# Kernel optimization log

Hardware: AMD Instinct MI355X
Metric: run time of the kernel (lower is better)

The kernel has to match this reference:

```python
import jax, jax.numpy as jnp
import numpy as np

DIM = 2048
H = 16        # num query heads
KVH = 4       # num kv heads
HD = DIM // H # head_dim = 128
RD = 64       # rope_dims (< head_dim -> partial rope)
BASE = 10000.0
SCALE = HD ** -0.5
EPS_RMS = 1e-6
EPS_NORM = 1e-12


def _rms_norm(x):
    return x * jax.lax.rsqrt(jnp.mean(x * x, axis=-1, keepdims=True) + EPS_RMS)


def _rope_cache(T):
    inv_freq = 1.0 / (BASE ** (jnp.arange(0, RD, 2, dtype=jnp.float32) / RD))  # [RD/2]
    t = jnp.arange(T, dtype=jnp.float32)
    freqs = t[:, None] * inv_freq[None, :]  # [T, RD/2]
    return jnp.cos(freqs)[None, None], jnp.sin(freqs)[None, None]  # [1,1,T,RD/2]


def _apply_rope(x, cos, sin):
    # x: [B, H, T, HD]; rotate first RD dims, pass through the rest
    x_rope, x_pass = x[..., :RD], x[..., RD:]
    half = RD // 2
    x1, x2 = x_rope[..., :half], x_rope[..., half:]
    x_rot = jnp.concatenate([x1 * cos - x2 * sin, x2 * cos + x1 * sin], axis=-1)
    return jnp.concatenate([x_rot, x_pass], axis=-1)


def setup_inputs() -> dict:
    key = jax.random.key(0)
    ks = jax.random.split(key, 6)
    x = jax.random.normal(ks[0], (4, 2048, DIM), dtype=jnp.float32)
    Wq = jax.random.normal(ks[1], (DIM, DIM), dtype=jnp.float32) * 0.02
    Wk = jax.random.normal(ks[2], (KVH * HD, DIM), dtype=jnp.float32) * 0.02
    Wv = jax.random.normal(ks[3], (KVH * HD, DIM), dtype=jnp.float32) * 0.02
    Wproj = jax.random.normal(ks[4], (DIM, DIM), dtype=jnp.float32) * 0.02
    q_gain = jnp.ones((H,), dtype=jnp.float32)
    return {"x": x, "Wq": Wq, "Wk": Wk, "Wv": Wv, "Wproj": Wproj, "q_gain": q_gain}


def reference(x, Wq, Wk, Wv, Wproj, q_gain):
    B, T, _ = x.shape
    # projections (nn.Linear: x @ W.T)  ->  [B, heads, T, HD]
    q = (x @ Wq.T).reshape(B, T, H, HD).transpose(0, 2, 1, 3)
    k = (x @ Wk.T).reshape(B, T, KVH, HD).transpose(0, 2, 1, 3)
    v = (x @ Wv.T).reshape(B, T, KVH, HD).transpose(0, 2, 1, 3)

    cos, sin = _rope_cache(T)
    q = _apply_rope(_rms_norm(q), cos, sin) * q_gain[None, :, None, None]
    k = _apply_rope(_rms_norm(k), cos, sin)

    # GQA: expand kv heads (kv head i serves query heads i*rep .. i*rep+rep-1)
    rep = H // KVH
    k = jnp.repeat(k, rep, axis=1)      # [B, H, T, HD]
    v_attn = jnp.repeat(v, rep, axis=1)  # [B, H, T, HD]

    # causal SDPA
    scores = jnp.einsum("bhqd,bhkd->bhqk", q, k) * SCALE
    causal = jnp.tril(jnp.ones((T, T), dtype=bool))
    scores = jnp.where(causal[None, None], scores, jnp.finfo(scores.dtype).min)
    attn = jax.nn.softmax(scores, axis=-1)
    y = jnp.einsum("bhqk,bhkd->bhqd", attn, v_attn)

    # xsa postproc: remove component of y along unit value direction
    vn = v_attn / jnp.maximum(
        jnp.linalg.norm(v_attn, axis=-1, keepdims=True), EPS_NORM)
    y = y - jnp.sum(y * vn, axis=-1, keepdims=True) * vn

    y = y.transpose(0, 2, 1, 3).reshape(B, T, DIM)
    return y @ Wproj.T
```

## Files before the change

kernel.cpp:

```cpp
#include <hip/hip_runtime.h>
#include <cstdint>
#include <cstddef>

typedef __bf16 bf16_t;
typedef __bf16 bf16x4 __attribute__((ext_vector_type(4)));
typedef __bf16 bf16x8 __attribute__((ext_vector_type(8)));
typedef float f32x4 __attribute__((ext_vector_type(4)));

#define B_ 4
#define T_ 2048
#define DIM_ 2048
#define H_ 16
#define KVH_ 4
#define HD_ 128
#define QKV_ 3072
#define QSCALE (0.08838834764831845f * 1.4426950408889634f)

__device__ __forceinline__ void gload16(const bf16_t* g, bf16_t* l) {
  __builtin_amdgcn_global_load_lds(
      (const __attribute__((address_space(1))) unsigned int*)g,
      (__attribute__((address_space(3))) unsigned int*)l, 16, 0, 0);
}

__global__ __launch_bounds__(256) void cvt_all(const float4* __restrict__ x,
                                               const float4* __restrict__ wq,
                                               const float4* __restrict__ wk,
                                               const float4* __restrict__ wv,
                                               const float4* __restrict__ wp,
                                               bf16x4* __restrict__ xb,
                                               bf16x4* __restrict__ wqkvb,
                                               bf16x4* __restrict__ wpb) {
  int i = blockIdx.x * 256 + threadIdx.x;
  const float4* s;
  bf16x4* dst;
  int off;
  if (i < 4194304) { s = x; dst = xb; off = i; }
  else if (i < 5242880) { s = wq; dst = wqkvb; off = i - 4194304; }
  else if (i < 5505024) { s = wk; dst = wqkvb + 1048576; off = i - 5242880; }
  else if (i < 5767168) { s = wv; dst = wqkvb + 1310720; off = i - 5505024; }
  else { s = wp; dst = wpb; off = i - 5767168; }
  float4 v = s[off];
  bf16x4 o = {(__bf16)v.x, (__bf16)v.y, (__bf16)v.z, (__bf16)v.w};
  dst[off] = o;
}

#define STAGE2(gsrc, ldst)                                   \
  do {                                                       \
    gload16((gsrc), (ldst) + tid * 8);                       \
    gload16((gsrc) + (size_t)128 * K, (ldst) + 4096 + tid * 8); \
  } while (0)

__global__ __launch_bounds__(512, 2) void gemm_bt(const bf16_t* __restrict__ A,
                                                  const bf16_t* __restrict__ B,
                                                  void* __restrict__ Cp,
                                                  int M, int N, int K, int out_bf16) {
  __shared__ __align__(16) bf16_t Ab[2 * 16384];
  __shared__ __align__(16) bf16_t Bb[2 * 16384];
  const int tid = threadIdx.x;
  const int w = tid >> 6, lane = tid & 63;
  const int m16 = lane & 15, q4 = lane >> 4;
  const int wr = w >> 2, wc = w & 3;
  const int rowBase = blockIdx.y * 256, colBase = blockIdx.x * 256;

  const int srow = tid >> 2, skc = tid & 3;
  const bf16_t* srcA = A + (size_t)(rowBase + srow) * K + (skc ^ (srow & 3)) * 8;
  const bf16_t* srcB = B + (size_t)(colBase + srow) * K + (skc ^ (srow & 3)) * 8;

  const int cs = (q4 ^ m16) & 3;
  const int aoff = wr * 4096 + m16 * 32 + cs * 8;
  const int boff = wc * 2048 + m16 * 32 + cs * 8;

  f32x4 acc[8][4];
#pragma unroll
  for (int i = 0; i < 8; ++i)
#pragma unroll
    for (int j = 0; j < 4; ++j) acc[i][j] = (f32x4){0.f, 0.f, 0.f, 0.f};

  const int nt = K >> 6;
  STAGE2(srcA, Ab);
  STAGE2(srcB, Bb);
  STAGE2(srcA + 32, Ab + 8192);
  STAGE2(srcB + 32, Bb + 8192);
  asm volatile("s_waitcnt vmcnt(4)" ::: "memory");
  __builtin_amdgcn_s_barrier();

#pragma unroll 1
  for (int t = 0; t < nt; ++t) {
    const int cb = (t & 1) << 14, nb = cb ^ 16384;
    const int pk = ((t + 1 < nt) ? t + 1 : t) << 6;
    const bf16_t* Ac = Ab + cb + aoff;
    const bf16_t* Bc = Bb + cb + boff;
    bf16x8 a[4], b[4];

    STAGE2(srcA + pk, Ab + nb);
#pragma unroll
    for (int i = 0; i < 4; ++i) a[i] = *(const bf16x8*)(Ac + i * 512);
#pragma unroll
    for (int j = 0; j < 4; ++j) b[j] = *(const bf16x8*)(Bc + j * 512);
    __builtin_amdgcn_s_barrier();
    asm volatile("s_waitcnt lgkmcnt(0)" ::: "memory");
    __builtin_amdgcn_sched_barrier(0);
    __builtin_amdgcn_s_setprio(1);
#pragma unroll
    for (int i = 0; i < 4; ++i)
#pragma unroll
      for (int j = 0; j < 4; ++j)
        acc[i][j] = __builtin_amdgcn_mfma_f32_16x16x32_bf16(a[i], b[j], acc[i][j], 0, 0, 0);
    __builtin_amdgcn_s_setprio(0);
    __builtin_amdgcn_s_barrier();

    STAGE2(srcB + pk, Bb + nb);
#pragma unroll
    for (int i = 0; i < 4; ++i) a[i] = *(const bf16x8*)(Ac + (4 + i) * 512);
    __builtin_amdgcn_s_barrier();
    asm volatile("s_waitcnt lgkmcnt(0)" ::: "memory");
    __builtin_amdgcn_sched_barrier(0);
    __builtin_amdgcn_s_setprio(1);
#pragma unroll
    for (int i = 0; i < 4; ++i)
#pragma unroll
      for (int j = 0; j < 4; ++j)
        acc[4 + i][j] = __builtin_amdgcn_mfma_f32_16x16x32_bf16(a[i], b[j], acc[4 + i][j], 0, 0, 0);
    __builtin_amdgcn_s_setprio(0);
    asm volatile("s_waitcnt vmcnt(4)" ::: "memory");
    __builtin_amdgcn_s_barrier();

    STAGE2(srcA + pk + 32, Ab + nb + 8192);
#pragma unroll
    for (int i = 0; i < 4; ++i) a[i] = *(const bf16x8*)(Ac + 8192 + i * 512);
#pragma unroll
    for (int j = 0; j < 4; ++j) b[j] = *(const bf16x8*)(Bc + 8192 + j * 512);
    __builtin_amdgcn_s_barrier();
    asm volatile("s_waitcnt lgkmcnt(0)" ::: "memory");
    __builtin_amdgcn_sched_barrier(0);
    __builtin_amdgcn_s_setprio(1);
#pragma unroll
    for (int i = 0; i < 4; ++i)
#pragma unroll
      for (int j = 0; j < 4; ++j)
        acc[i][j] = __builtin_amdgcn_mfma_f32_16x16x32_bf16(a[i], b[j], acc[i][j], 0, 0, 0);
    __builtin_amdgcn_s_setprio(0);
    __builtin_amdgcn_s_barrier();

    STAGE2(srcB + pk + 32, Bb + nb + 8192);
#pragma unroll
    for (int i = 0; i < 4; ++i) a[i] = *(const bf16x8*)(Ac + 8192 + (4 + i) * 512);
    __builtin_amdgcn_s_barrier();
    asm volatile("s_waitcnt lgkmcnt(0)" ::: "memory");
    __builtin_amdgcn_sched_barrier(0);
    __builtin_amdgcn_s_setprio(1);
#pragma unroll
    for (int i = 0; i < 4; ++i)
#pragma unroll
      for (int j = 0; j < 4; ++j)
        acc[4 + i][j] = __builtin_amdgcn_mfma_f32_16x16x32_bf16(a[i], b[j], acc[4 + i][j], 0, 0, 0);
    __builtin_amdgcn_s_setprio(0);
    asm volatile("s_waitcnt vmcnt(4)" ::: "memory");
    __builtin_amdgcn_s_barrier();
  }

  if (out_bf16) {
    bf16_t* C = (bf16_t*)Cp;
#pragma unroll
    for (int i = 0; i < 8; ++i)
#pragma unroll
      for (int j = 0; j < 4; ++j)
#pragma unroll
        for (int r = 0; r < 4; ++r) {
          int row = rowBase + wr * 128 + i * 16 + q4 * 4 + r;
          int col = colBase + wc * 64 + j * 16 + m16;
          C[(size_t)row * N + col] = (bf16_t)acc[i][j][r];
        }
  } else {
    float* C = (float*)Cp;
#pragma unroll
    for (int i = 0; i < 8; ++i)
#pragma unroll
      for (int j = 0; j < 4; ++j)
#pragma unroll
        for (int r = 0; r < 4; ++r) {
          int row = rowBase + wr * 128 + i * 16 + q4 * 4 + r;
          int col = colBase + wc * 64 + j * 16 + m16;
          C[(size_t)row * N + col] = acc[i][j][r];
        }
  }
}

__global__ __launch_bounds__(256) void gemm_qkv(const bf16_t* __restrict__ A,
                                                const bf16_t* __restrict__ Bw,
                                                bf16_t* __restrict__ qkv,
                                                bf16_t* __restrict__ vt,
                                                const float* __restrict__ gain) {
  __shared__ bf16_t As[128 * 32];
  __shared__ bf16_t Bs[128 * 32];
  __shared__ float ssbuf[2][128];
  const int tid = threadIdx.x;
  const int w = tid >> 6, lane = tid & 63;
  const int m = lane & 15, quad = lane >> 4;
  const int wr = w >> 1, wc = w & 1;
  const int rowBase = blockIdx.y * 128, colBase = blockIdx.x * 128;

  f32x4 acc[4][4];
#pragma unroll
  for (int i = 0; i < 4; ++i)
#pragma unroll
    for (int j = 0; j < 4; ++j) acc[i][j] = (f32x4){0.f, 0.f, 0.f, 0.f};

  for (int kk = 0; kk < 64; ++kk) {
    const int k0 = kk << 5;
#pragma unroll
    for (int i2 = 0; i2 < 2; ++i2) {
      int idx = i2 * 256 + tid;
      int row = idx >> 2, kc = idx & 3;
      gload16(A + (size_t)(rowBase + row) * 2048 + k0 + kc * 8, &As[idx * 8]);
      gload16(Bw + (size_t)(colBase + row) * 2048 + k0 + kc * 8, &Bs[idx * 8]);
    }
    __syncthreads();
    bf16x8 a[4], bb[4];
#pragma unroll
    for (int i = 0; i < 4; ++i)
      a[i] = *(const bf16x8*)&As[(wr * 64 + i * 16 + m) * 32 + quad * 8];
#pragma unroll
    for (int j = 0; j < 4; ++j)
      bb[j] = *(const bf16x8*)&Bs[(wc * 64 + j * 16 + m) * 32 + quad * 8];
#pragma unroll
    for (int i = 0; i < 4; ++i)
#pragma unroll
      for (int j = 0; j < 4; ++j)
        acc[i][j] = __builtin_amdgcn_mfma_f32_16x16x32_bf16(a[i], bb[j], acc[i][j], 0, 0, 0);
    __syncthreads();
  }

  const int bx = blockIdx.x;
  if (bx < 20) {
    const float g = (bx < 16) ? gain[bx] * QSCALE : 1.0f;
#pragma unroll
    for (int i = 0; i < 4; ++i) {
      float ssp[4];
#pragma unroll
      for (int r = 0; r < 4; ++r) {
        float s = 0.f;
#pragma unroll
        for (int j = 0; j < 4; ++j) s += acc[i][j][r] * acc[i][j][r];
#pragma unroll
        for (int off = 1; off <= 8; off <<= 1) s += __shfl_xor(s, off);
        ssp[r] = s;
      }
      if (m == 0) {
#pragma unroll
        for (int r = 0; r < 4; ++r) ssbuf[wc][wr * 64 + i * 16 + quad * 4 + r] = ssp[r];
      }
    }
    __syncthreads();
    const float if0 = exp2f(-(float)m * 0.4152410118609203f);
    const float if1 = exp2f(-(float)(16 + m) * 0.4152410118609203f);
#pragma unroll
    for (int i = 0; i < 4; ++i) {
#pragma unroll
      for (int r = 0; r < 4; ++r) {
        const int ridx = wr * 64 + i * 16 + quad * 4 + r;
        const int row = rowBase + ridx;
        const float rn = rsqrtf((ssbuf[0][ridx] + ssbuf[1][ridx]) * (1.f / 128.f) + 1e-6f);
        float v0 = acc[i][0][r] * rn, v1 = acc[i][1][r] * rn;
        float v2 = acc[i][2][r] * rn, v3 = acc[i][3][r] * rn;
        float o0 = v0, o1 = v1, o2 = v2, o3 = v3;
        if (wc == 0) {
          const float t = (float)(row & (T_ - 1));
          const float a0 = t * if0, a1 = t * if1;
          const float c0_ = cosf(a0), s0_ = sinf(a0);
          const float c1_ = cosf(a1), s1_ = sinf(a1);
          o0 = v0 * c0_ - v2 * s0_;
          o1 = v1 * c1_ - v3 * s1_;
          o2 = v2 * c0_ + v0 * s0_;
          o3 = v3 * c1_ + v1 * s1_;
        }
        bf16_t* out = qkv + (size_t)row * QKV_ + colBase + wc * 64 + m;
        out[0]  = (bf16_t)(o0 * g);
        out[16] = (bf16_t)(o1 * g);
        out[32] = (bf16_t)(o2 * g);
        out[48] = (bf16_t)(o3 * g);
      }
    }
  } else {
    const int kvh = bx - 20;
#pragma unroll
    for (int i = 0; i < 4; ++i)
#pragma unroll
      for (int j = 0; j < 4; ++j) {
        const int row0 = rowBase + wr * 64 + i * 16 + quad * 4;
        const int d = wc * 64 + j * 16 + m;
        bf16x4 pv;
#pragma unroll
        for (int r = 0; r < 4; ++r) {
          pv[r] = (bf16_t)acc[i][j][r];
          qkv[(size_t)(row0 + r) * QKV_ + colBase + d] = pv[r];
        }
        const int b = row0 >> 11, t0 = row0 & (T_ - 1);
        *(bf16x4*)(vt + ((size_t)(b * KVH_ + kvh) * HD_ + d) * T_ + t0) = pv;
      }
  }
}

__global__ __launch_bounds__(256) void attn_kernel(const bf16_t* __restrict__ qkv,
                                                   const bf16_t* __restrict__ vt,
                                                   bf16_t* __restrict__ y) {
  __shared__ __align__(16) bf16_t Ks[2][32 * 128];
  __shared__ __align__(16) bf16_t Vs[2][128 * 32];
  __shared__ __align__(16) bf16_t Ps[4][32 * 40];

  const int tid = threadIdx.x;
  const int w = tid >> 6, lane = tid & 63;
  const int m = lane & 15, q = lane >> 4;
  const int h = blockIdx.y, b = blockIdx.z, kvh = h >> 2;

  const bf16_t* qptr = qkv + (size_t)(b * T_) * QKV_ + h * HD_;
  const bf16_t* kptr = qkv + (size_t)(b * T_) * QKV_ + DIM_ + kvh * HD_;
  const bf16_t* vptr = qkv + (size_t)(b * T_) * QKV_ + DIM_ + KVH_ * HD_ + kvh * HD_;
  const bf16_t* vtptr = vt + (size_t)(b * KVH_ + kvh) * HD_ * T_;

  const int kKey0 = tid >> 4, kC0 = tid & 15;
  const int kKey1 = (256 + tid) >> 4, kC1 = tid & 15;
  const int vD0 = tid >> 2, vC0 = tid & 3;
  const int vD1 = (256 + tid) >> 2, vC1 = tid & 3;
  const int vS0 = (vD0 ^ (vD0 >> 2)) & 3, vS1 = (vD1 ^ (vD1 >> 2)) & 3;

  int koff[2][4], voff[8], poff[2];
#pragma unroll
  for (int kf = 0; kf < 2; ++kf)
#pragma unroll
    for (int c = 0; c < 4; ++c)
      koff[kf][c] = (kf * 16 + m) * 128 + (((c * 4 + q) ^ m) & 15) * 8;
#pragma unroll
  for (int f = 0; f < 8; ++f) {
    const int d = f * 16 + m;
    voff[f] = d * 32 + ((q ^ ((d ^ (d >> 2)) & 3)) & 3) * 8;
  }
#pragma unroll
  for (int qf = 0; qf < 2; ++qf) poff[qf] = (qf * 16 + m) * 40 + q * 8;

#pragma unroll 1
  for (int ti = 0; ti < 2; ++ti) {
    const int qb = ((ti == 0) ? (15 - (int)blockIdx.x) : (int)blockIdx.x) * 128;
    const int qbw = qb + w * 32;
    const int nk = (qb >> 5) + 4;

    bf16x8 aq[2][4];
#pragma unroll
    for (int qf = 0; qf < 2; ++qf)
#pragma unroll
      for (int c = 0; c < 4; ++c)
        aq[qf][c] = *(const bf16x8*)(qptr + (size_t)(qbw + qf * 16 + m) * QKV_ + c * 32 + q * 8);

    f32x4 o[2][8];
#pragma unroll
    for (int qf = 0; qf < 2; ++qf)
#pragma unroll
      for (int f = 0; f < 8; ++f) o[qf][f] = (f32x4){0.f, 0.f, 0.f, 0.f};
    float l_r[2] = {0.f, 0.f};

    {
      gload16(kptr + (size_t)kKey0 * QKV_ + ((kC0 ^ kKey0) & 15) * 8, &Ks[0][tid * 8]);
      gload16(kptr + (size_t)kKey1 * QKV_ + ((kC1 ^ kKey1) & 15) * 8, &Ks[0][(256 + tid) * 8]);
      gload16(vtptr + (size_t)vD0 * T_ + (vC0 ^ vS0) * 8, &Vs[0][tid * 8]);
      gload16(vtptr + (size_t)vD1 * T_ + (vC1 ^ vS1) * 8, &Vs[0][(256 + tid) * 8]);
    }

#pragma unroll 1
    for (int it = 0; it < nk; ++it) {
      const int kb = it << 5;
      __syncthreads();

      if (it + 1 < nk) {
        const int kb2 = kb + 32;
        bf16_t* Kb = Ks[(it + 1) & 1];
        bf16_t* Vb = Vs[(it + 1) & 1];
        gload16(kptr + (size_t)(kb2 + kKey0) * QKV_ + ((kC0 ^ kKey0) & 15) * 8, &Kb[tid * 8]);
        gload16(kptr + (size_t)(kb2 + kKey1) * QKV_ + ((kC1 ^ kKey1) & 15) * 8, &Kb[(256 + tid) * 8]);
        gload16(vtptr + (size_t)vD0 * T_ + kb2 + (vC0 ^ vS0) * 8, &Vb[tid * 8]);
        gload16(vtptr + (size_t)vD1 * T_ + kb2 + (vC1 ^ vS1) * 8, &Vb[(256 + tid) * 8]);
      }

      if (kb > qbw + 31) continue;
      const bf16_t* Kb = Ks[it & 1];
      const bf16_t* Vb = Vs[it & 1];

      f32x4 S[2][2];
#pragma unroll
      for (int qf = 0; qf < 2; ++qf)
#pragma unroll
        for (int kf = 0; kf < 2; ++kf) S[qf][kf] = (f32x4){0.f, 0.f, 0.f, 0.f};
#pragma unroll
      for (int kf = 0; kf < 2; ++kf)
#pragma unroll
        for (int c = 0; c < 4; ++c) {
          bf16x8 ak = *(const bf16x8*)&Kb[koff[kf][c]];
          S[0][kf] = __builtin_amdgcn_mfma_f32_16x16x32_bf16(ak, aq[0][c], S[0][kf], 0, 0, 0);
          S[1][kf] = __builtin_amdgcn_mfma_f32_16x16x32_bf16(ak, aq[1][c], S[1][kf], 0, 0, 0);
        }

      const bool needmask = (kb + 31) > qbw;
#pragma unroll
      for (int qf = 0; qf < 2; ++qf) {
        const int qrow = qbw + qf * 16 + m;
        if (needmask) {
#pragma unroll
          for (int kf = 0; kf < 2; ++kf)
#pragma unroll
            for (int r = 0; r < 4; ++r) {
              int key = kb + kf * 16 + q * 4 + r;
              if (key > qrow) S[qf][kf][r] = -1e30f;
            }
        }
        float rs = 0.f;
#pragma unroll
        for (int kf = 0; kf < 2; ++kf)
#pragma unroll
          for (int r = 0; r < 4; ++r) {
            float p = exp2f(S[qf][kf][r]);
            S[qf][kf][r] = p;
            rs += p;
          }
        rs += __shfl_xor(rs, 16);
        rs += __shfl_xor(rs, 32);
        l_r[qf] += rs;
#pragma unroll
        for (int kf = 0; kf < 2; ++kf) {
          bf16x4 pk = {(__bf16)S[qf][kf][0], (__bf16)S[qf][kf][1],
                       (__bf16)S[qf][kf][2], (__bf16)S[qf][kf][3]};
          *(bf16x4*)&Ps[w][(qf * 16 + m) * 40 + kf * 16 + q * 4] = pk;
        }
      }
      asm volatile("s_waitcnt lgkmcnt(0)" ::: "memory");

      bf16x8 Pb[2];
#pragma unroll
      for (int qf = 0; qf < 2; ++qf)
        Pb[qf] = *(const bf16x8*)&Ps[w][poff[qf]];
#pragma unroll
      for (int f = 0; f < 8; ++f) {
        bf16x8 av = *(const bf16x8*)&Vb[voff[f]];
        o[0][f] = __builtin_amdgcn_mfma_f32_16x16x32_bf16(av, Pb[0], o[0][f], 0, 0, 0);
        o[1][f] = __builtin_amdgcn_mfma_f32_16x16x32_bf16(av, Pb[1], o[1][f], 0, 0, 0);
      }
    }

#pragma unroll
    for (int qf = 0; qf < 2; ++qf) {
      const int trow = qbw + qf * 16 + m;
      const float linv = 1.f / l_r[qf];
      bf16x4 vv[8];
      float n2 = 0.f, dp = 0.f;
#pragma unroll
      for (int f = 0; f < 8; ++f) {
        vv[f] = *(const bf16x4*)(vptr + (size_t)trow * QKV_ + f * 16 + q * 4);
#pragma unroll
        for (int r = 0; r < 4; ++r) {
          float v = (float)vv[f][r];
          n2 += v * v;
          dp += o[qf][f][r] * linv * v;
        }
      }
      n2 += __shfl_xor(n2, 16); n2 += __shfl_xor(n2, 32);
      dp += __shfl_xor(dp, 16); dp += __shfl_xor(dp, 32);
      float d = fmaxf(sqrtf(n2), 1e-12f);
      float coef = dp / (d * d);
#pragma unroll
      for (int f = 0; f < 8; ++f) {
        bf16x4 yo;
#pragma unroll
        for (int r = 0; r < 4; ++r)
          yo[r] = (bf16_t)(o[qf][f][r] * linv - coef * (float)vv[f][r]);
        *(bf16x4*)(y + (size_t)(b * T_ + trow) * DIM_ + h * HD_ + f * 16 + q * 4) = yo;
      }
    }
    __syncthreads();
  }
}

extern "C" void kernel_launch(void* const* d_in, const int* in_sizes, int n_in,
                              void* d_out, int out_size, void* d_ws, size_t ws_size,
                              hipStream_t stream) {
  const float* x = (const float*)d_in[0];
  const float* Wq = (const float*)d_in[1];
  const float* Wk = (const float*)d_in[2];
  const float* Wv = (const float*)d_in[3];
  const float* Wp = (const float*)d_in[4];
  const float* qg = (const float*)d_in[5];

  bf16_t* xbf = (bf16_t*)d_ws;
  bf16_t* wqkv = xbf + (size_t)8192 * 2048;
  bf16_t* wproj = wqkv + (size_t)3072 * 2048;
  bf16_t* qkv = wproj + (size_t)2048 * 2048;
  bf16_t* vt = qkv + (size_t)8192 * 3072;
  bf16_t* ybf = xbf;

  cvt_all<<<26624, 256, 0, stream>>>((const float4*)x, (const float4*)Wq,
                                     (const float4*)Wk, (const float4*)Wv,
                                     (const float4*)Wp, (bf16x4*)xbf,
                                     (bf16x4*)wqkv, (bf16x4*)wproj);
  gemm_qkv<<<dim3(24, 64), 256, 0, stream>>>(xbf, wqkv, qkv, vt, qg);
  attn_kernel<<<dim3(8, 16, 4), 256, 0, stream>>>(qkv, vt, ybf);
  gemm_bt<<<dim3(8, 32), 512, 0, stream>>>(ybf, wproj, d_out, 8192, 2048, 2048, 0);
}
```

Baseline: 546.9 us.

## Port QKV GEMM to 256x256 pipelined tile and strengthen LDS swizzle

Replaces the simple 128x128 single-buffered QKV GEMM with the 512-thread, 256x256, double-buffered, prioritised MFMA pipeline already used for the output projection. The RMSnorm, RoPE and V-transpose epilogue is remapped so each block now covers two heads. It also adds an extra XOR term to the LDS swizzle in both GEMMs to reduce bank conflicts. The goal is more data reuse per block and overlap of global loads with MFMA, at the cost of more registers and LDS per block and fewer blocks in the grid.

```diff
diff --git a/kernel.cpp b/kernel.cpp
--- a/kernel.cpp
+++ b/kernel.cpp
@@ -44,10 +44,10 @@
   dst[off] = o;
 }
 
-#define STAGE2(gsrc, ldst)                                   \
-  do {                                                       \
-    gload16((gsrc), (ldst) + tid * 8);                       \
-    gload16((gsrc) + (size_t)128 * K, (ldst) + 4096 + tid * 8); \
+#define STAGE2(gsrc, ldst, KK)                                  \
+  do {                                                          \
+    gload16((gsrc), (ldst) + tid * 8);                          \
+    gload16((gsrc) + (size_t)128 * (KK), (ldst) + 4096 + tid * 8); \
   } while (0)
 
 __global__ __launch_bounds__(512, 2) void gemm_bt(const bf16_t* __restrict__ A,
@@ -63,10 +63,11 @@
   const int rowBase = blockIdx.y * 256, colBase = blockIdx.x * 256;
 
   const int srow = tid >> 2, skc = tid & 3;
-  const bf16_t* srcA = A + (size_t)(rowBase + srow) * K + (skc ^ (srow & 3)) * 8;
-  const bf16_t* srcB = B + (size_t)(colBase + srow) * K + (skc ^ (srow & 3)) * 8;
-
-  const int cs = (q4 ^ m16) & 3;
+  const int sswz = (skc ^ (srow & 3) ^ ((srow >> 2) & 3)) & 3;
+  const bf16_t* srcA = A + (size_t)(rowBase + srow) * K + sswz * 8;
+  const bf16_t* srcB = B + (size_t)(colBase + srow) * K + sswz * 8;
+
+  const int cs = (q4 ^ (m16 & 3) ^ ((m16 >> 2) & 3)) & 3;
   const int aoff = wr * 4096 + m16 * 32 + cs * 8;
   const int boff = wc * 2048 + m16 * 32 + cs * 8;
 
@@ -77,10 +78,10 @@
     for (int j = 0; j < 4; ++j) acc[i][j] = (f32x4){0.f, 0.f, 0.f, 0.f};
 
   const int nt = K >> 6;
-  STAGE2(srcA, Ab);
-  STAGE2(srcB, Bb);
-  STAGE2(srcA + 32, Ab + 8192);
-  STAGE2(srcB + 32, Bb + 8192);
+  STAGE2(srcA, Ab, K);
+  STAGE2(srcB, Bb, K);
+  STAGE2(srcA + 32, Ab + 8192, K);
+  STAGE2(srcB + 32, Bb + 8192, K);
   asm volatile("s_waitcnt vmcnt(4)" ::: "memory");
   __builtin_amdgcn_s_barrier();
 
@@ -92,7 +93,7 @@
     const bf16_t* Bc = Bb + cb + boff;
     bf16x8 a[4], b[4];
 
-    STAGE2(srcA + pk, Ab + nb);
+    STAGE2(srcA + pk, Ab + nb, K);
 #pragma unroll
     for (int i = 0; i < 4; ++i) a[i] = *(const bf16x8*)(Ac + i * 512);
 #pragma unroll
@@ -109,7 +110,7 @@
     __builtin_amdgcn_s_setprio(0);
     __builtin_amdgcn_s_barrier();
 
-    STAGE2(srcB + pk, Bb + nb);
+    STAGE2(srcB + pk, Bb + nb, K);
 #pragma unroll
     for (int i = 0; i < 4; ++i) a[i] = *(const bf16x8*)(Ac + (4 + i) * 512);
     __builtin_amdgcn_s_barrier();
@@ -125,7 +126,7 @@
     asm volatile("s_waitcnt vmcnt(4)" ::: "memory");
     __builtin_amdgcn_s_barrier();
 
-    STAGE2(srcA + pk + 32, Ab + nb + 8192);
+    STAGE2(srcA + pk + 32, Ab + nb + 8192, K);
 #pragma unroll
     for (int i = 0; i < 4; ++i) a[i] = *(const bf16x8*)(Ac + 8192 + i * 512);
 #pragma unroll
@@ -142,7 +143,7 @@
     __builtin_amdgcn_s_setprio(0);
     __builtin_amdgcn_s_barrier();
 
-    STAGE2(srcB + pk + 32, Bb + nb + 8192);
+    STAGE2(srcB + pk + 32, Bb + nb + 8192, K);
 #pragma unroll
     for (int i = 0; i < 4; ++i) a[i] = *(const bf16x8*)(Ac + 8192 + (4 + i) * 512);
     __builtin_amdgcn_s_barrier();
@@ -186,85 +187,148 @@
   }
 }
 
-__global__ __launch_bounds__(256) void gemm_qkv(const bf16_t* __restrict__ A,
-                                                const bf16_t* __restrict__ Bw,
-                                                bf16_t* __restrict__ qkv,
-                                                bf16_t* __restrict__ vt,
-                                                const float* __restrict__ gain) {
-  __shared__ bf16_t As[128 * 32];
-  __shared__ bf16_t Bs[128 * 32];
-  __shared__ float ssbuf[2][128];
+__global__ __launch_bounds__(512, 2) void gemm_qkv(const bf16_t* __restrict__ A,
+                                                   const bf16_t* __restrict__ Bw,
+                                                   bf16_t* __restrict__ qkv,
+                                                   bf16_t* __restrict__ vt,
+                                                   const float* __restrict__ gain) {
+  __shared__ __align__(16) bf16_t Ab[2 * 16384];
+  __shared__ __align__(16) bf16_t Bb[2 * 16384];
+  __shared__ float ssbuf[4][256];
   const int tid = threadIdx.x;
   const int w = tid >> 6, lane = tid & 63;
-  const int m = lane & 15, quad = lane >> 4;
-  const int wr = w >> 1, wc = w & 1;
-  const int rowBase = blockIdx.y * 128, colBase = blockIdx.x * 128;
-
-  f32x4 acc[4][4];
-#pragma unroll
-  for (int i = 0; i < 4; ++i)
+  const int m16 = lane & 15, q4 = lane >> 4;
+  const int wr = w >> 2, wc = w & 3;
+  const int rowBase = blockIdx.y * 256, colBase = blockIdx.x * 256;
+
+  const int srow = tid >> 2, skc = tid & 3;
+  const int sswz = (skc ^ (srow & 3) ^ ((srow >> 2) & 3)) & 3;
+  const bf16_t* srcA = A + (size_t)(rowBase + srow) * 2048 + sswz * 8;
+  const bf16_t* srcB = Bw + (size_t)(colBase + srow) * 2048 + sswz * 8;
+
+  const int cs = (q4 ^ (m16 & 3) ^ ((m16 >> 2) & 3)) & 3;
+  const int aoff = wr * 4096 + m16 * 32 + cs * 8;
+  const int boff = wc * 2048 + m16 * 32 + cs * 8;
+
+  f32x4 acc[8][4];
+#pragma unroll
+  for (int i = 0; i < 8; ++i)
 #pragma unroll
     for (int j = 0; j < 4; ++j) acc[i][j] = (f32x4){0.f, 0.f, 0.f, 0.f};
 
-  for (int kk = 0; kk < 64; ++kk) {
-    const int k0 = kk << 5;
-#pragma unroll
-    for (int i2 = 0; i2 < 2; ++i2) {
-      int idx = i2 * 256 + tid;
-      int row = idx >> 2, kc = idx & 3;
-      gload16(A + (size_t)(rowBase + row) * 2048 + k0 + kc * 8, &As[idx * 8]);
-      gload16(Bw + (size_t)(colBase + row) * 2048 + k0 + kc * 8, &Bs[idx * 8]);
+  STAGE2(srcA, Ab, 2048);
+  STAGE2(srcB, Bb, 2048);
+  STAGE2(srcA + 32, Ab + 8192, 2048);
+  STAGE2(srcB + 32, Bb + 8192, 2048);
+  asm volatile("s_waitcnt vmcnt(4)" ::: "memory");
+  __builtin_amdgcn_s_barrier();
+
+#pragma unroll 1
+  for (int t = 0; t < 32; ++t) {
+    const int cb = (t & 1) << 14, nb = cb ^ 16384;
+    const int pk = ((t + 1 < 32) ? t + 1 : t) << 6;
+    const bf16_t* Ac = Ab + cb + aoff;
+    const bf16_t* Bc = Bb + cb + boff;
+    bf16x8 a[4], b[4];
+
+    STAGE2(srcA + pk, Ab + nb, 2048);
+#pragma unroll
+    for (int i = 0; i < 4; ++i) a[i] = *(const bf16x8*)(Ac + i * 512);
+#pragma unroll
+    for (int j = 0; j < 4; ++j) b[j] = *(const bf16x8*)(Bc + j * 512);
+    __builtin_amdgcn_s_barrier();
+    asm volatile("s_waitcnt lgkmcnt(0)" ::: "memory");
+    __builtin_amdgcn_sched_barrier(0);
+    __builtin_amdgcn_s_setprio(1);
+#pragma unroll
+    for (int i = 0; i < 4; ++i)
+#pragma unroll
+      for (int j = 0; j < 4; ++j)
+        acc[i][j] = __builtin_amdgcn_mfma_f32_16x16x32_bf16(a[i], b[j], acc[i][j], 0, 0, 0);
+    __builtin_amdgcn_s_setprio(0);
+    __builtin_amdgcn_s_barrier();
+
+    STAGE2(srcB + pk, Bb + nb, 2048);
+#pragma unroll
+    for (int i = 0; i < 4; ++i) a[i] = *(const bf16x8*)(Ac + (4 + i) * 512);
+    __builtin_amdgcn_s_barrier();
+    asm volatile("s_waitcnt lgkmcnt(0)" ::: "memory");
+    __builtin_amdgcn_sched_barrier(0);
+    __builtin_amdgcn_s_setprio(1);
+#pragma unroll
+    for (int i = 0; i < 4; ++i)
+#pragma unroll
+      for (int j = 0; j < 4; ++j)
+        acc[4 + i][j] = __builtin_amdgcn_mfma_f32_16x16x32_bf16(a[i], b[j], acc[4 + i][j], 0, 0, 0);
+    __builtin_amdgcn_s_setprio(0);
+    asm volatile("s_waitcnt vmcnt(4)" ::: "memory");
+    __builtin_amdgcn_s_barrier();
+
+    STAGE2(srcA + pk + 32, Ab + nb + 8192, 2048);
+#pragma unroll
+    for (int i = 0; i < 4; ++i) a[i] = *(const bf16x8*)(Ac + 8192 + i * 512);
+#pragma unroll
+    for (int j = 0; j < 4; ++j) b[j] = *(const bf16x8*)(Bc + 8192 + j * 512);
+    __builtin_amdgcn_s_barrier();
+    asm volatile("s_waitcnt lgkmcnt(0)" ::: "memory");
+    __builtin_amdgcn_sched_barrier(0);
+    __builtin_amdgcn_s_setprio(1);
+#pragma unroll
+    for (int i = 0; i < 4; ++i)
+#pragma unroll
+      for (int j = 0; j < 4; ++j)
+        acc[i][j] = __builtin_amdgcn_mfma_f32_16x16x32_bf16(a[i], b[j], acc[i][j], 0, 0, 0);
+    __builtin_amdgcn_s_setprio(0);
+    __builtin_amdgcn_s_barrier();
+
+    STAGE2(srcB + pk + 32, Bb + nb + 8192, 2048);
+#pragma unroll
+    for (int i = 0; i < 4; ++i) a[i] = *(const bf16x8*)(Ac + 8192 + (4 + i) * 512);
+    __builtin_amdgcn_s_barrier();
+    asm volatile("s_waitcnt lgkmcnt(0)" ::: "memory");
+    __builtin_amdgcn_sched_barrier(0);
+    __builtin_amdgcn_s_setprio(1);
+#pragma unroll
+    for (int i = 0; i < 4; ++i)
+#pragma unroll
+      for (int j = 0; j < 4; ++j)
+        acc[4 + i][j] = __builtin_amdgcn_mfma_f32_16x16x32_bf16(a[i], b[j], acc[4 + i][j], 0, 0, 0);
+    __builtin_amdgcn_s_setprio(0);
+    asm volatile("s_waitcnt vmcnt(4)" ::: "memory");
+    __builtin_amdgcn_s_barrier();
+  }
+
+  const int bx = blockIdx.x;
+  if (bx < 10) {
+    const int h = bx * 2 + (wc >> 1);
+    const float g = (bx < 8) ? gain[h] * QSCALE : 1.0f;
+#pragma unroll
+    for (int i = 0; i < 8; ++i) {
+#pragma unroll
+      for (int r = 0; r < 4; ++r) {
+        float s = 0.f;
+#pragma unroll
+        for (int j = 0; j < 4; ++j) s += acc[i][j][r] * acc[i][j][r];
+#pragma unroll
+        for (int off = 1; off <= 8; off <<= 1) s += __shfl_xor(s, off);
+        if (m16 == 0) ssbuf[wc][wr * 128 + i * 16 + q4 * 4 + r] = s;
+      }
     }
     __syncthreads();
-    bf16x8 a[4], bb[4];
-#pragma unroll
-    for (int i = 0; i < 4; ++i)
-      a[i] = *(const bf16x8*)&As[(wr * 64 + i * 16 + m) * 32 + quad * 8];
-#pragma unroll
-    for (int j = 0; j < 4; ++j)
-      bb[j] = *(const bf16x8*)&Bs[(wc * 64 + j * 16 + m) * 32 + quad * 8];
-#pragma unroll
-    for (int i = 0; i < 4; ++i)
-#pragma unroll
-      for (int j = 0; j < 4; ++j)
-        acc[i][j] = __builtin_amdgcn_mfma_f32_16x16x32_bf16(a[i], bb[j], acc[i][j], 0, 0, 0);
-    __syncthreads();
-  }
-
-  const int bx = blockIdx.x;
-  if (bx < 20) {
-    const float g = (bx < 16) ? gain[bx] * QSCALE : 1.0f;
-#pragma unroll
-    for (int i = 0; i < 4; ++i) {
-      float ssp[4];
+    const float if0 = exp2f(-(float)m16 * 0.4152410118609203f);
+    const float if1 = exp2f(-(float)(16 + m16) * 0.4152410118609203f);
+#pragma unroll
+    for (int i = 0; i < 8; ++i) {
 #pragma unroll
       for (int r = 0; r < 4; ++r) {
-        float s = 0.f;
-#pragma unroll
-        for (int j = 0; j < 4; ++j) s += acc[i][j][r] * acc[i][j][r];
-#pragma unroll
-        for (int off = 1; off <= 8; off <<= 1) s += __shfl_xor(s, off);
-        ssp[r] = s;
-      }
-      if (m == 0) {
-#pragma unroll
-        for (int r = 0; r < 4; ++r) ssbuf[wc][wr * 64 + i * 16 + quad * 4 + r] = ssp[r];
-      }
-    }
-    __syncthreads();
-    const float if0 = exp2f(-(float)m * 0.4152410118609203f);
-    const float if1 = exp2f(-(float)(16 + m) * 0.4152410118609203f);
-#pragma unroll
-    for (int i = 0; i < 4; ++i) {
-#pragma unroll
-      for (int r = 0; r < 4; ++r) {
-        const int ridx = wr * 64 + i * 16 + quad * 4 + r;
+        const int ridx = wr * 128 + i * 16 + q4 * 4 + r;
         const int row = rowBase + ridx;
-        const float rn = rsqrtf((ssbuf[0][ridx] + ssbuf[1][ridx]) * (1.f / 128.f) + 1e-6f);
+        const float rn =
+            rsqrtf((ssbuf[wc & 2][ridx] + ssbuf[(wc & 2) | 1][ridx]) * (1.f / 128.f) + 1e-6f);
         float v0 = acc[i][0][r] * rn, v1 = acc[i][1][r] * rn;
         float v2 = acc[i][2][r] * rn, v3 = acc[i][3][r] * rn;
         float o0 = v0, o1 = v1, o2 = v2, o3 = v3;
-        if (wc == 0) {
+        if ((wc & 1) == 0) {
           const float t = (float)(row & (T_ - 1));
           const float a0 = t * if0, a1 = t * if1;
           const float c0_ = cosf(a0), s0_ = sinf(a0);
@@ -274,7 +338,7 @@
           o2 = v2 * c0_ + v0 * s0_;
           o3 = v3 * c1_ + v1 * s1_;
         }
-        bf16_t* out = qkv + (size_t)row * QKV_ + colBase + wc * 64 + m;
+        bf16_t* out = qkv + (size_t)row * QKV_ + colBase + wc * 64 + m16;
         out[0]  = (bf16_t)(o0 * g);
         out[16] = (bf16_t)(o1 * g);
         out[32] = (bf16_t)(o2 * g);
@@ -282,18 +346,18 @@
       }
     }
   } else {
-    const int kvh = bx - 20;
-#pragma unroll
-    for (int i = 0; i < 4; ++i)
+    const int kvh = (bx - 10) * 2 + (wc >> 1);
+#pragma unroll
+    for (int i = 0; i < 8; ++i)
 #pragma unroll
       for (int j = 0; j < 4; ++j) {
-        const int row0 = rowBase + wr * 64 + i * 16 + quad * 4;
-        const int d = wc * 64 + j * 16 + m;
+        const int row0 = rowBase + wr * 128 + i * 16 + q4 * 4;
+        const int d = (wc & 1) * 64 + j * 16 + m16;
         bf16x4 pv;
 #pragma unroll
         for (int r = 0; r < 4; ++r) {
           pv[r] = (bf16_t)acc[i][j][r];
-          qkv[(size_t)(row0 + r) * QKV_ + colBase + d] = pv[r];
+          qkv[(size_t)(row0 + r) * QKV_ + colBase + wc * 64 + j * 16 + m16] = pv[r];
         }
         const int b = row0 >> 11, t0 = row0 & (T_ - 1);
         *(bf16x4*)(vt + ((size_t)(b * KVH_ + kvh) * HD_ + d) * T_ + t0) = pv;
@@ -498,7 +562,7 @@
                                      (const float4*)Wk, (const float4*)Wv,
                                      (const float4*)Wp, (bf16x4*)xbf,
                                      (bf16x4*)wqkv, (bf16x4*)wproj);
-  gemm_qkv<<<dim3(24, 64), 256, 0, stream>>>(xbf, wqkv, qkv, vt, qg);
+  gemm_qkv<<<dim3(12, 32), 512, 0, stream>>>(xbf, wqkv, qkv, vt, qg);
   attn_kernel<<<dim3(8, 16, 4), 256, 0, stream>>>(qkv, vt, ybf);
   gemm_bt<<<dim3(8, 32), 512, 0, stream>>>(ybf, wproj, d_out, 8192, 2048, 2048, 0);
 }
```

New measurement: 618.4 us. 13.1% more time.
